# Kernel optimization log

Measured on AMD Instinct MI355X. Metric: run time of the kernel, lower is better.

## Reference

```python
import jax, jax.numpy as jnp
import numpy as np

B, L, D = 4, 4096, 256


def setup_inputs() -> dict:
    key = jax.random.key(0)
    k_x, k_q, k_k, k_v, k_w, k_b = jax.random.split(key, 6)
    s = 1.0 / np.sqrt(D)
    return {
        "x": jax.random.normal(k_x, (B, L, D), dtype=jnp.float32),
        "Wq": jax.random.normal(k_q, (D, D), dtype=jnp.float32) * s,   # nn.Linear weight (out,in)
        "Wk": jax.random.normal(k_k, (D, D), dtype=jnp.float32) * s,
        "Wv": jax.random.normal(k_v, (D, D), dtype=jnp.float32) * s,
        "w_mlp": jax.random.normal(k_w, (D,), dtype=jnp.float32) * s,  # Linear(D,1) weight
        "b_mlp": jnp.zeros((), dtype=jnp.float32),                     # Linear(D,1) bias
    }


def reference(x, Wq, Wk, Wv, w_mlp, b_mlp):
    # Projections (nn.Linear: y = x @ W.T, no bias)
    Q = jnp.einsum("bld,ed->ble", x, Wq)
    K = jnp.einsum("bld,ed->ble", x, Wk)
    V = jnp.einsum("bld,ed->ble", x, Wv)
    # score[b,i,j] = relu((Q[b,i]-K[b,j]) @ w_mlp + b_mlp)
    # decomposed: (Q-K)@w = Q@w - K@w  (exact same math, no (B,L,L,D) tensor)
    q_s = Q @ w_mlp  # (B,L)
    k_s = K @ w_mlp  # (B,L)
    scores = jax.nn.relu(q_s[:, :, None] - k_s[:, None, :] + b_mlp)  # (B,L,L)
    attn = jax.nn.softmax(scores, axis=-1)  # softmax over key axis j
    # out[b,i,d] = sum_j attn[b,i,j] * V[b,j,d]
    out = jnp.einsum("bij,bjd->bid", attn, V)
    return out  # dropout p=0.0 is identity
```

## Files before the change

### kernel.cpp

```cpp
#include <hip/hip_runtime.h>
#include <math.h>

#define BB 4
#define LL 4096
#define DD 256
#define NROWS (BB*LL)
#define CHUNK 32
#define NC (LL/CHUNK)
#define NB 8192

__global__ void k_uvec(const float* __restrict__ Wq, const float* __restrict__ Wk,
                       const float* __restrict__ w, float* __restrict__ u) {
    __shared__ float wl[DD];
    int d = threadIdx.x;
    wl[d] = w[d];
    __syncthreads();
    float aq = 0.f, ak = 0.f;
    #pragma unroll 8
    for (int e = 0; e < DD; ++e) {
        float we = wl[e];
        aq = fmaf(Wq[e*DD + d], we, aq);
        ak = fmaf(Wk[e*DD + d], we, ak);
    }
    u[d] = aq;
    u[DD + d] = ak;
}

__global__ void k_proj(const float* __restrict__ x, const float* __restrict__ u,
                       const float* __restrict__ bmlp,
                       float* __restrict__ a, float* __restrict__ c) {
    int row = blockIdx.x * 4 + (threadIdx.x >> 6);
    int lane = threadIdx.x & 63;
    float4 xv = ((const float4*)(x + (size_t)row * DD))[lane];
    float4 uq = ((const float4*)u)[lane];
    float4 uk = ((const float4*)(u + DD))[lane];
    float sq = xv.x*uq.x + xv.y*uq.y + xv.z*uq.z + xv.w*uq.w;
    float sk = xv.x*uk.x + xv.y*uk.y + xv.z*uk.z + xv.w*uk.w;
    #pragma unroll
    for (int off = 32; off > 0; off >>= 1) {
        sq += __shfl_down(sq, off);
        sk += __shfl_down(sk, off);
    }
    if (lane == 0) {
        a[row] = sq + bmlp[0];
        c[row] = sk;
    }
}

__global__ void __launch_bounds__(1024) k_sortish(const float* __restrict__ c,
        int* __restrict__ binstart_g,
        int* __restrict__ perm,
        float* __restrict__ c_sorted, float* __restrict__ e_sorted,
        float* __restrict__ SE,
        float* __restrict__ hdr) {
    __shared__ float cl[LL];
    __shared__ int   hist[NB];
    __shared__ float esl[LL];
    __shared__ float scrf[64];
    int b = blockIdx.x, tid = threadIdx.x;
    int wave = tid >> 6, lane = tid & 63;
    int* scri = (int*)scrf;

    float4 cv = ((const float4*)(c + (size_t)b*LL))[tid];
    ((float4*)cl)[tid] = cv;
    float cw[4] = {cv.x, cv.y, cv.z, cv.w};
    float mn = fminf(fminf(cw[0],cw[1]), fminf(cw[2],cw[3]));
    float mx = fmaxf(fmaxf(cw[0],cw[1]), fmaxf(cw[2],cw[3]));
    #pragma unroll
    for (int off = 32; off > 0; off >>= 1) {
        mn = fminf(mn, __shfl_down(mn, off));
        mx = fmaxf(mx, __shfl_down(mx, off));
    }
    if (lane == 0) { scrf[wave] = mn; scrf[32 + wave] = mx; }
    __syncthreads();
    if (wave == 0) {
        float m = (lane < 16) ? scrf[lane]      :  3.4e38f;
        float M = (lane < 16) ? scrf[32 + lane] : -3.4e38f;
        #pragma unroll
        for (int off = 32; off > 0; off >>= 1) {
            m = fminf(m, __shfl_down(m, off));
            M = fmaxf(M, __shfl_down(M, off));
        }
        if (lane == 0) { scrf[0] = m; scrf[1] = M; }
    }
    __syncthreads();
    float cmin = scrf[0], cmax = scrf[1];
    float scale = (float)NB / fmaxf(cmax - cmin, 1e-20f);
    __syncthreads();

    ((int4*)hist)[tid] = make_int4(0,0,0,0);
    ((int4*)hist)[tid + 1024] = make_int4(0,0,0,0);
    __syncthreads();

    int bins[4];
    #pragma unroll
    for (int u = 0; u < 4; ++u) {
        int bi = (int)((cw[u] - cmin) * scale);
        bi = bi < 0 ? 0 : (bi > NB-1 ? NB-1 : bi);
        bins[u] = bi;
        atomicAdd(&hist[bi], 1);
    }
    __syncthreads();

    int loc[8]; int base = 0;
    #pragma unroll
    for (int j = 0; j < 8; ++j) { loc[j] = base; base += hist[tid*8 + j]; }
    int incl = base;
    #pragma unroll
    for (int off = 1; off < 64; off <<= 1) {
        int t = __shfl_up(incl, off);
        if (lane >= off) incl += t;
    }
    if (lane == 63) scri[wave] = incl;
    __syncthreads();
    if (wave == 0) {
        int v = (lane < 16) ? scri[lane] : 0;
        int s = v;
        #pragma unroll
        for (int off = 1; off < 16; off <<= 1) {
            int t = __shfl_up(s, off);
            if (lane >= off) s += t;
        }
        if (lane < 16) scri[lane] = s - v;
    }
    __syncthreads();
    int thread_excl = (incl - base) + scri[wave];
    __syncthreads();
    #pragma unroll
    for (int j = 0; j < 8; ++j) {
        int bs = thread_excl + loc[j];
        binstart_g[(size_t)b*(NB+2) + tid*8 + j] = bs;
        hist[tid*8 + j] = bs;
    }
    if (tid == 0) {
        binstart_g[(size_t)b*(NB+2) + NB]     = LL;
        binstart_g[(size_t)b*(NB+2) + NB + 1] = LL;
        hdr[b*2 + 0] = cmin;
        hdr[b*2 + 1] = scale;
    }
    __syncthreads();

    #pragma unroll
    for (int u = 0; u < 4; ++u) {
        int i = tid*4 + u;
        int r = atomicAdd(&hist[bins[u]], 1);
        float e = expf(cmin - cw[u]);
        perm[(size_t)b*LL + r] = i;
        c_sorted[(size_t)b*LL + r] = cw[u];
        e_sorted[(size_t)b*LL + r] = e;
        esl[r] = e;
    }
    __syncthreads();

    float le[4]; float s0 = 0.f;
    #pragma unroll
    for (int u = 0; u < 4; ++u) { le[u] = s0; s0 += esl[tid*4 + u]; }
    float fincl = s0;
    #pragma unroll
    for (int off = 1; off < 64; off <<= 1) {
        float t = __shfl_up(fincl, off);
        if (lane >= off) fincl += t;
    }
    if (lane == 63) scrf[wave] = fincl;
    __syncthreads();
    if (wave == 0) {
        float v = (lane < 16) ? scrf[lane] : 0.f;
        float s = v;
        #pragma unroll
        for (int off = 1; off < 16; off <<= 1) {
            float t = __shfl_up(s, off);
            if (lane >= off) s += t;
        }
        if (lane < 16) scrf[lane] = s - v;
    }
    __syncthreads();
    float texcl = (fincl - s0) + scrf[wave];
    #pragma unroll
    for (int u = 0; u < 4; ++u)
        SE[(size_t)b*(LL+1) + tid*4 + u] = texcl + le[u];
    if (tid == 1023) SE[(size_t)b*(LL+1) + LL] = texcl + s0;
}

__global__ void __launch_bounds__(256) k_gemm_v(const float* __restrict__ x,
        const float* __restrict__ Wv, float* __restrict__ V) {
    __shared__ float4 As[64*9];
    __shared__ float4 Bs[128*9];
    const int tid = threadIdx.x;
    const int rowBase = blockIdx.x * 64;
    const int colBase = blockIdx.y * 128;
    const int ty = tid >> 4;
    const int tx = tid & 15;

    float acc[4][8];
    #pragma unroll
    for (int r = 0; r < 4; ++r)
        #pragma unroll
        for (int s = 0; s < 8; ++s) acc[r][s] = 0.f;

    for (int k0 = 0; k0 < DD; k0 += 32) {
        __syncthreads();
        #pragma unroll
        for (int rep = 0; rep < 2; ++rep) {
            int idx = tid + 256*rep;
            int m = idx >> 3, kc = idx & 7;
            As[m*9 + kc] = *(const float4*)(x + (size_t)(rowBase + m) * DD + k0 + 4*kc);
        }
        #pragma unroll
        for (int rep = 0; rep < 4; ++rep) {
            int idx = tid + 256*rep;
            int n = idx >> 3, kc = idx & 7;
            Bs[n*9 + kc] = *(const float4*)(Wv + (size_t)(colBase + n) * DD + k0 + 4*kc);
        }
        __syncthreads();
        #pragma unroll
        for (int kc = 0; kc < 8; ++kc) {
            float4 af[4], bf[8];
            #pragma unroll
            for (int r = 0; r < 4; ++r) af[r] = As[(ty + 16*r)*9 + kc];
            #pragma unroll
            for (int s = 0; s < 8; ++s) bf[s] = Bs[(tx + 16*s)*9 + kc];
            #pragma unroll
            for (int r = 0; r < 4; ++r)
                #pragma unroll
                for (int s = 0; s < 8; ++s) {
                    acc[r][s] = fmaf(af[r].x, bf[s].x, acc[r][s]);
                    acc[r][s] = fmaf(af[r].y, bf[s].y, acc[r][s]);
                    acc[r][s] = fmaf(af[r].z, bf[s].z, acc[r][s]);
                    acc[r][s] = fmaf(af[r].w, bf[s].w, acc[r][s]);
                }
        }
    }
    #pragma unroll
    for (int r = 0; r < 4; ++r) {
        size_t rowo = (size_t)(rowBase + ty + 16*r) * DD + colBase;
        #pragma unroll
        for (int s = 0; s < 8; ++s)
            V[rowo + tx + 16*s] = acc[r][s];
    }
}

__global__ void k_scan(const float* __restrict__ V, const int* __restrict__ perm,
        const float* __restrict__ e_sorted,
        float* __restrict__ Pl, float* __restrict__ Pel,
        float* __restrict__ Tp, float* __restrict__ Te) {
    int b = blockIdx.y, q = blockIdx.x;
    int d = threadIdx.x;
    __shared__ int pj[CHUNK];
    __shared__ float pe[CHUNK];
    if (d < CHUNK) {
        pj[d] = perm[(size_t)b*LL + q*CHUNK + d];
        pe[d] = e_sorted[(size_t)b*LL + q*CHUNK + d];
    }
    __syncthreads();
    float vr[CHUNK];
    #pragma unroll
    for (int r = 0; r < CHUNK; ++r)
        vr[r] = V[((size_t)b*LL + pj[r]) * DD + d];
    float acc = 0.f, acce = 0.f;
    size_t kb = (size_t)b*LL + (size_t)q*CHUNK;
    #pragma unroll
    for (int r = 0; r < CHUNK; ++r) {
        size_t o = (kb + r) * DD + d;
        Pl[o]  = acc;
        Pel[o] = acce;
        acc += vr[r];
        acce = fmaf(pe[r], vr[r], acce);
    }
    size_t to = ((size_t)b*NC + q) * DD + d;
    Tp[to] = acc;
    Te[to] = acce;
}

__global__ void k_base(const float* __restrict__ Tp, const float* __restrict__ Te,
        float* __restrict__ baseP, float* __restrict__ basePe) {
    int b = blockIdx.x, d = threadIdx.x;
    float acc = 0.f, acce = 0.f;
    #pragma unroll 16
    for (int q = 0; q < NC; ++q) {
        size_t o = ((size_t)b*(NC+1) + q) * DD + d;
        baseP[o] = acc; basePe[o] = acce;
        size_t ti = ((size_t)b*NC + q) * DD + d;
        acc += Tp[ti]; acce += Te[ti];
    }
    size_t o = ((size_t)b*(NC+1) + NC) * DD + d;
    baseP[o] = acc; basePe[o] = acce;
}

__global__ void k_out(const float* __restrict__ a, const float* __restrict__ hdr,
                      const int* __restrict__ binstart,
                      const float* __restrict__ c_sorted, const float* __restrict__ e_sorted,
                      const int* __restrict__ perm, const float* __restrict__ V,
                      const float* __restrict__ SE,
                      const float* __restrict__ Pl, const float* __restrict__ Pel,
                      const float* __restrict__ baseP, const float* __restrict__ basePe,
                      float* __restrict__ out) {
    int row = blockIdx.x * 4 + (threadIdx.x >> 6);
    int lane = threadIdx.x & 63;
    int b = row >> 12;
    float ai = a[row];
    float cmin = hdr[b*2 + 0], scale = hdr[b*2 + 1];
    float t = (ai - cmin) * scale;
    int ib = t < 0.f ? 0 : (t >= (float)NB ? NB : (int)t);
    int k    = binstart[(size_t)b*(NB+2) + ib];
    int kend = binstart[(size_t)b*(NB+2) + ib + 1];
    float alpha = expf(cmin - ai);
    float Z = fmaf(alpha, (float)(LL - k), SE[(size_t)b*(LL+1) + k]);
    size_t db = (size_t)lane * 4;
    size_t totoff = ((size_t)b * (NC+1) + NC) * DD + db;
    float4 ptot  = *(const float4*)(baseP  + totoff);
    float4 pk, pek;
    if (k < LL) {
        int q = k >> 5;
        size_t po = ((size_t)b * LL + k) * DD + db;
        size_t bo = ((size_t)b * (NC+1) + q) * DD + db;
        float4 pl = *(const float4*)(Pl    + po);
        float4 bp = *(const float4*)(baseP + bo);
        float4 pe = *(const float4*)(Pel    + po);
        float4 be = *(const float4*)(basePe + bo);
        pk.x = pl.x + bp.x; pk.y = pl.y + bp.y; pk.z = pl.z + bp.z; pk.w = pl.w + bp.w;
        pek.x = pe.x + be.x; pek.y = pe.y + be.y; pek.z = pe.z + be.z; pek.w = pe.w + be.w;
    } else {
        pk = ptot;
        float4 pt = *(const float4*)(basePe + totoff);
        pek = pt;
    }
    float4 num;
    num.x = fmaf(alpha, ptot.x - pk.x, pek.x);
    num.y = fmaf(alpha, ptot.y - pk.y, pek.y);
    num.z = fmaf(alpha, ptot.z - pk.z, pek.z);
    num.w = fmaf(alpha, ptot.w - pk.w, pek.w);
    for (int r = k; r < kend; ++r) {
        float cr = c_sorted[(size_t)b*LL + r];
        if (cr < ai) {
            float w = e_sorted[(size_t)b*LL + r] - alpha;
            int j = perm[(size_t)b*LL + r];
            float4 v = *(const float4*)(V + ((size_t)b*LL + j) * DD + db);
            num.x = fmaf(w, v.x, num.x);
            num.y = fmaf(w, v.y, num.y);
            num.z = fmaf(w, v.z, num.z);
            num.w = fmaf(w, v.w, num.w);
            Z += w;
        }
    }
    float invZ = 1.f / Z;
    float4 o;
    o.x = num.x * invZ; o.y = num.y * invZ; o.z = num.z * invZ; o.w = num.w * invZ;
    *(float4*)(out + (size_t)row * DD + db) = o;
}

extern "C" void kernel_launch(void* const* d_in, const int* in_sizes, int n_in,
                              void* d_out, int out_size, void* d_ws, size_t ws_size,
                              hipStream_t stream) {
    const float* x  = (const float*)d_in[0];
    const float* Wq = (const float*)d_in[1];
    const float* Wk = (const float*)d_in[2];
    const float* Wv = (const float*)d_in[3];
    const float* wm = (const float*)d_in[4];
    const float* bm = (const float*)d_in[5];
    float* out = (float*)d_out;
    float* ws = (float*)d_ws;

    size_t off = 0;
    auto alloc = [&](size_t n) {
        float* p = ws + off;
        off += (n + 255) & ~(size_t)255;
        return p;
    };
    float* u        = alloc(2*DD);
    float* a        = alloc(NROWS);
    float* c        = alloc(NROWS);
    float* c_sorted = alloc(NROWS);
    float* e_sorted = alloc(NROWS);
    float* SE       = alloc((size_t)BB*(LL+1));
    int*   perm     = (int*)alloc(NROWS);
    int*   binstart = (int*)alloc((size_t)BB*(NB+2));
    float* hdr      = alloc(2*BB);
    float* V        = alloc((size_t)NROWS*DD);
    float* Pl       = alloc((size_t)NROWS*DD);
    float* Pel      = alloc((size_t)NROWS*DD);
    float* Tp       = alloc((size_t)BB*NC*DD);
    float* Te       = alloc((size_t)BB*NC*DD);
    float* baseP    = alloc((size_t)BB*(NC+1)*DD);
    float* basePe   = alloc((size_t)BB*(NC+1)*DD);

    hipLaunchKernelGGL(k_uvec, dim3(1), dim3(DD), 0, stream, Wq, Wk, wm, u);
    hipLaunchKernelGGL(k_proj, dim3(NROWS/4), dim3(256), 0, stream, x, u, bm, a, c);
    hipLaunchKernelGGL(k_sortish, dim3(BB), dim3(1024), 0, stream,
                       c, binstart, perm, c_sorted, e_sorted, SE, hdr);
    hipLaunchKernelGGL(k_gemm_v, dim3(NROWS/64, DD/128), dim3(256), 0, stream, x, Wv, V);
    hipLaunchKernelGGL(k_scan, dim3(NC, BB), dim3(DD), 0, stream, V, perm, e_sorted, Pl, Pel, Tp, Te);
    hipLaunchKernelGGL(k_base, dim3(BB), dim3(DD), 0, stream, Tp, Te, baseP, basePe);
    hipLaunchKernelGGL(k_out, dim3(NROWS/4), dim3(256), 0, stream,
                       a, hdr, binstart, c_sorted, e_sorted, perm, V,
                       SE, Pl, Pel, baseP, basePe, out);
}
```

Measured before the change: 165.6 us.

## Fuse score projections into V GEMM and split u-vector reduction across blocks

Removes the separate k_proj pass by computing the per-row q and k scalar projections inside the V GEMM blocks with blockIdx.y==0, reusing the x tiles already staged in shared memory. The u-vector kernel now runs across 16 blocks that combine partial sums with atomicAdd, which needs a memset first, instead of one serial block. The GEMM tile width shrinks from 128 to 64 columns, giving twice as many blocks. The aim is to avoid a second full read of x and one launch, at the cost of extra work in a quarter of the GEMM blocks and float atomics that make u's summation order nondeterministic.

```diff
diff --git a/kernel.cpp b/kernel.cpp
--- a/kernel.cpp
+++ b/kernel.cpp
@@ -11,39 +11,110 @@
 
 __global__ void k_uvec(const float* __restrict__ Wq, const float* __restrict__ Wk,
                        const float* __restrict__ w, float* __restrict__ u) {
-    __shared__ float wl[DD];
+    __shared__ float wl[16];
     int d = threadIdx.x;
-    wl[d] = w[d];
+    int e0 = blockIdx.x * 16;
+    if (d < 16) wl[d] = w[e0 + d];
     __syncthreads();
     float aq = 0.f, ak = 0.f;
-    #pragma unroll 8
-    for (int e = 0; e < DD; ++e) {
-        float we = wl[e];
-        aq = fmaf(Wq[e*DD + d], we, aq);
-        ak = fmaf(Wk[e*DD + d], we, ak);
-    }
-    u[d] = aq;
-    u[DD + d] = ak;
-}
-
-__global__ void k_proj(const float* __restrict__ x, const float* __restrict__ u,
-                       const float* __restrict__ bmlp,
-                       float* __restrict__ a, float* __restrict__ c) {
-    int row = blockIdx.x * 4 + (threadIdx.x >> 6);
-    int lane = threadIdx.x & 63;
-    float4 xv = ((const float4*)(x + (size_t)row * DD))[lane];
-    float4 uq = ((const float4*)u)[lane];
-    float4 uk = ((const float4*)(u + DD))[lane];
-    float sq = xv.x*uq.x + xv.y*uq.y + xv.z*uq.z + xv.w*uq.w;
-    float sk = xv.x*uk.x + xv.y*uk.y + xv.z*uk.z + xv.w*uk.w;
-    #pragma unroll
-    for (int off = 32; off > 0; off >>= 1) {
-        sq += __shfl_down(sq, off);
-        sk += __shfl_down(sk, off);
-    }
-    if (lane == 0) {
-        a[row] = sq + bmlp[0];
-        c[row] = sk;
+    #pragma unroll
+    for (int j = 0; j < 16; ++j) {
+        float we = wl[j];
+        aq = fmaf(Wq[(size_t)(e0 + j)*DD + d], we, aq);
+        ak = fmaf(Wk[(size_t)(e0 + j)*DD + d], we, ak);
+    }
+    atomicAdd(&u[d], aq);
+    atomicAdd(&u[DD + d], ak);
+}
+
+__global__ void __launch_bounds__(256) k_gemm_v(const float* __restrict__ x,
+        const float* __restrict__ Wv, const float* __restrict__ u,
+        const float* __restrict__ bmlp,
+        float* __restrict__ V, float* __restrict__ a, float* __restrict__ c) {
+    __shared__ float4 As[64*9];
+    __shared__ float4 Bs[64*9];
+    __shared__ float4 ul[128];
+    __shared__ float prosq[256];
+    __shared__ float prosk[256];
+    const int tid = threadIdx.x;
+    const int rowBase = blockIdx.x * 64;
+    const int colBase = blockIdx.y * 64;
+    const int ty = tid >> 4;
+    const int tx = tid & 15;
+    const int pr = tid & 63;
+    const int pq = tid >> 6;
+
+    if (tid < 128) ul[tid] = ((const float4*)u)[tid];
+
+    float acc[4][4];
+    #pragma unroll
+    for (int r = 0; r < 4; ++r)
+        #pragma unroll
+        for (int s = 0; s < 4; ++s) acc[r][s] = 0.f;
+    float aq = 0.f, ak = 0.f;
+
+    for (int k0 = 0; k0 < DD; k0 += 32) {
+        __syncthreads();
+        #pragma unroll
+        for (int rep = 0; rep < 2; ++rep) {
+            int idx = tid + 256*rep;
+            int m = idx >> 3, kc = idx & 7;
+            As[m*9 + kc] = *(const float4*)(x + (size_t)(rowBase + m) * DD + k0 + 4*kc);
+        }
+        #pragma unroll
+        for (int rep = 0; rep < 2; ++rep) {
+            int idx = tid + 256*rep;
+            int n = idx >> 3, kc = idx & 7;
+            Bs[n*9 + kc] = *(const float4*)(Wv + (size_t)(colBase + n) * DD + k0 + 4*kc);
+        }
+        __syncthreads();
+        if (blockIdx.y == 0) {
+            #pragma unroll
+            for (int h = 0; h < 2; ++h) {
+                int kc = pq*2 + h;
+                float4 av = As[pr*9 + kc];
+                float4 q4 = ul[(k0 >> 2) + kc];
+                float4 k4 = ul[64 + (k0 >> 2) + kc];
+                aq = fmaf(av.x, q4.x, fmaf(av.y, q4.y, fmaf(av.z, q4.z, fmaf(av.w, q4.w, aq))));
+                ak = fmaf(av.x, k4.x, fmaf(av.y, k4.y, fmaf(av.z, k4.z, fmaf(av.w, k4.w, ak))));
+            }
+        }
+        #pragma unroll
+        for (int kc = 0; kc < 8; ++kc) {
+            float4 af[4], bf[4];
+            #pragma unroll
+            for (int r = 0; r < 4; ++r) af[r] = As[(ty + 16*r)*9 + kc];
+            #pragma unroll
+            for (int s = 0; s < 4; ++s) bf[s] = Bs[(tx + 16*s)*9 + kc];
+            #pragma unroll
+            for (int r = 0; r < 4; ++r)
+                #pragma unroll
+                for (int s = 0; s < 4; ++s) {
+                    acc[r][s] = fmaf(af[r].x, bf[s].x, acc[r][s]);
+                    acc[r][s] = fmaf(af[r].y, bf[s].y, acc[r][s]);
+                    acc[r][s] = fmaf(af[r].z, bf[s].z, acc[r][s]);
+                    acc[r][s] = fmaf(af[r].w, bf[s].w, acc[r][s]);
+                }
+        }
+    }
+    #pragma unroll
+    for (int r = 0; r < 4; ++r) {
+        size_t rowo = (size_t)(rowBase + ty + 16*r) * DD + colBase;
+        #pragma unroll
+        for (int s = 0; s < 4; ++s)
+            V[rowo + tx + 16*s] = acc[r][s];
+    }
+    if (blockIdx.y == 0) {
+        __syncthreads();
+        prosq[pq*64 + pr] = aq;
+        prosk[pq*64 + pr] = ak;
+        __syncthreads();
+        if (tid < 64) {
+            float sa = prosq[tid] + prosq[64+tid] + prosq[128+tid] + prosq[192+tid];
+            float sc = prosk[tid] + prosk[64+tid] + prosk[128+tid] + prosk[192+tid];
+            a[rowBase + tid] = sa + bmlp[0];
+            c[rowBase + tid] = sc;
+        }
     }
 }
 
@@ -179,64 +250,6 @@
     for (int u = 0; u < 4; ++u)
         SE[(size_t)b*(LL+1) + tid*4 + u] = texcl + le[u];
     if (tid == 1023) SE[(size_t)b*(LL+1) + LL] = texcl + s0;
-}
-
-__global__ void __launch_bounds__(256) k_gemm_v(const float* __restrict__ x,
-        const float* __restrict__ Wv, float* __restrict__ V) {
-    __shared__ float4 As[64*9];
-    __shared__ float4 Bs[128*9];
-    const int tid = threadIdx.x;
-    const int rowBase = blockIdx.x * 64;
-    const int colBase = blockIdx.y * 128;
-    const int ty = tid >> 4;
-    const int tx = tid & 15;
-
-    float acc[4][8];
-    #pragma unroll
-    for (int r = 0; r < 4; ++r)
-        #pragma unroll
-        for (int s = 0; s < 8; ++s) acc[r][s] = 0.f;
-
-    for (int k0 = 0; k0 < DD; k0 += 32) {
-        __syncthreads();
-        #pragma unroll
-        for (int rep = 0; rep < 2; ++rep) {
-            int idx = tid + 256*rep;
-            int m = idx >> 3, kc = idx & 7;
-            As[m*9 + kc] = *(const float4*)(x + (size_t)(rowBase + m) * DD + k0 + 4*kc);
-        }
-        #pragma unroll
-        for (int rep = 0; rep < 4; ++rep) {
-            int idx = tid + 256*rep;
-            int n = idx >> 3, kc = idx & 7;
-            Bs[n*9 + kc] = *(const float4*)(Wv + (size_t)(colBase + n) * DD + k0 + 4*kc);
-        }
-        __syncthreads();
-        #pragma unroll
-        for (int kc = 0; kc < 8; ++kc) {
-            float4 af[4], bf[8];
-            #pragma unroll
-            for (int r = 0; r < 4; ++r) af[r] = As[(ty + 16*r)*9 + kc];
-            #pragma unroll
-            for (int s = 0; s < 8; ++s) bf[s] = Bs[(tx + 16*s)*9 + kc];
-            #pragma unroll
-            for (int r = 0; r < 4; ++r)
-                #pragma unroll
-                for (int s = 0; s < 8; ++s) {
-                    acc[r][s] = fmaf(af[r].x, bf[s].x, acc[r][s]);
-                    acc[r][s] = fmaf(af[r].y, bf[s].y, acc[r][s]);
-                    acc[r][s] = fmaf(af[r].z, bf[s].z, acc[r][s]);
-                    acc[r][s] = fmaf(af[r].w, bf[s].w, acc[r][s]);
-                }
-        }
-    }
-    #pragma unroll
-    for (int r = 0; r < 4; ++r) {
-        size_t rowo = (size_t)(rowBase + ty + 16*r) * DD + colBase;
-        #pragma unroll
-        for (int s = 0; s < 8; ++s)
-            V[rowo + tx + 16*s] = acc[r][s];
-    }
 }
 
 __global__ void k_scan(const float* __restrict__ V, const int* __restrict__ perm,
@@ -383,11 +396,12 @@
     float* baseP    = alloc((size_t)BB*(NC+1)*DD);
     float* basePe   = alloc((size_t)BB*(NC+1)*DD);
 
-    hipLaunchKernelGGL(k_uvec, dim3(1), dim3(DD), 0, stream, Wq, Wk, wm, u);
-    hipLaunchKernelGGL(k_proj, dim3(NROWS/4), dim3(256), 0, stream, x, u, bm, a, c);
+    hipMemsetAsync(u, 0, 2*DD*sizeof(float), stream);
+    hipLaunchKernelGGL(k_uvec, dim3(16), dim3(DD), 0, stream, Wq, Wk, wm, u);
+    hipLaunchKernelGGL(k_gemm_v, dim3(NROWS/64, DD/64), dim3(256), 0, stream,
+                       x, Wv, u, bm, V, a, c);
     hipLaunchKernelGGL(k_sortish, dim3(BB), dim3(1024), 0, stream,
                        c, binstart, perm, c_sorted, e_sorted, SE, hdr);
-    hipLaunchKernelGGL(k_gemm_v, dim3(NROWS/64, DD/128), dim3(256), 0, stream, x, Wv, V);
     hipLaunchKernelGGL(k_scan, dim3(NC, BB), dim3(DD), 0, stream, V, perm, e_sorted, Pl, Pel, Tp, Te);
     hipLaunchKernelGGL(k_base, dim3(BB), dim3(DD), 0, stream, Tp, Te, baseP, basePe);
     hipLaunchKernelGGL(k_out, dim3(NROWS/4), dim3(256), 0, stream,
```

Measured after the change: 148.6 us. 1.11x faster.
